# Kernel optimization log

Measured on AMD Instinct MI355X. Metric: run time of the kernel, lower is better.

Reference implementation:

```python
import jax, jax.numpy as jnp
import numpy as np

L, B, T, C, H, FF = 2, 2, 2048, 512, 8, 1024
HS = C // H  # head size
EPS = 1.1920929e-07  # torch float32 finfo eps (nn.RMSNorm default)


def setup_inputs() -> dict:
    key = jax.random.key(0)
    ks = jax.random.split(key, 20)
    s = 0.02
    return {
        "hidden": jax.random.normal(ks[0], (B, T, C), jnp.float32),
        "target": jax.random.normal(ks[1], (B, T, C), jnp.float32),
        # self-attn per-head projections (bias=False)
        "Wq_s": jax.random.normal(ks[2], (L, H, C, HS)) * s,
        "Wk_s": jax.random.normal(ks[3], (L, H, C, HS)) * s,
        "Wv_s": jax.random.normal(ks[4], (L, H, C, HS)) * s,
        "Wo_s": jax.random.normal(ks[5], (L, C, C)) * s,
        "bo_s": jnp.zeros((L, C)),
        # cross-attn per-head projections
        "Wq_x": jax.random.normal(ks[6], (L, H, C, HS)) * s,
        "Wk_x": jax.random.normal(ks[7], (L, H, C, HS)) * s,
        "Wv_x": jax.random.normal(ks[8], (L, H, C, HS)) * s,
        "Wo_x": jax.random.normal(ks[9], (L, C, C)) * s,
        "bo_x": jnp.zeros((L, C)),
        # FFN
        "W1": jax.random.normal(ks[10], (L, C, FF)) * s,
        "b1": jnp.zeros((L, FF)),
        "W2": jax.random.normal(ks[11], (L, FF, C)) * s,
        "b2": jnp.zeros((L, C)),
        # RMSNorm gains ln1..ln4
        "g1": jnp.ones((L, C)),
        "g2": jnp.ones((L, C)),
        "g3": jnp.ones((L, C)),
        "g4": jnp.ones((L, C)),
    }


def _rms(x, g):
    return x * jax.lax.rsqrt(jnp.mean(x * x, axis=-1, keepdims=True) + EPS) * g


def _attn(q_in, kv_in, Wq, Wk, Wv, Wo, bo, causal):
    # q_in: [B,Tq,C], kv_in: [B,Tk,C]; W*: [H,C,HS]
    q = jnp.einsum('btc,hcd->bhtd', q_in, Wq)
    k = jnp.einsum('bsc,hcd->bhsd', kv_in, Wk)
    v = jnp.einsum('bsc,hcd->bhsd', kv_in, Wv)
    wei = jnp.einsum('bhtd,bhsd->bhts', q, k) * (HS ** -0.5)  # [B,H,Tq,Tk]
    if causal:
        Tq, Tk = q_in.shape[1], kv_in.shape[1]
        mask = jnp.tril(jnp.ones((Tq, Tk), bool))
        wei = jnp.where(mask, wei, -jnp.inf)
    wei = jax.nn.softmax(wei, axis=-1)
    out = jnp.einsum('bhts,bhsd->bhtd', wei, v)
    out = out.transpose(0, 2, 1, 3).reshape(q_in.shape[0], q_in.shape[1], C)
    return out @ Wo + bo


def reference(hidden, target, Wq_s, Wk_s, Wv_s, Wo_s, bo_s,
              Wq_x, Wk_x, Wv_x, Wo_x, bo_x,
              W1, b1, W2, b2, g1, g2, g3, g4):
    t = target
    for l in range(L):
        # masked self-attention with RMSNorm pre-norm + residual
        t = t + _attn(_rms(t, g1[l]), _rms(t, g1[l]), Wq_s[l], Wk_s[l], Wv_s[l],
                      Wo_s[l], bo_s[l], causal=True)
        # cross-attention: K/V from ln2(hidden), Q from ln3(t)
        t = t + _attn(_rms(t, g3[l]), _rms(hidden, g2[l]), Wq_x[l], Wk_x[l], Wv_x[l],
                      Wo_x[l], bo_x[l], causal=False)
        # GELU FFN
        h = _rms(t, g4[l])
        t = t + (jax.nn.gelu(h @ W1[l] + b1[l], approximate=False) @ W2[l] + b2[l])
    return t
```

## Files before the change

### kernel.cpp

```cpp
#include <hip/hip_runtime.h>
#include <hip/hip_bf16.h>
#include <math.h>

#define L 2
#define B 2
#define T 2048
#define C 512
#define H 8
#define FF 1024
#define HS 64
#define EPSV 1.1920929e-07f

typedef __hip_bfloat16 bf16;
typedef __attribute__((ext_vector_type(8))) short short8;
typedef __attribute__((ext_vector_type(4))) float f32x4;

__device__ __forceinline__ float b2f(bf16 x) { return __bfloat162float(x); }

__device__ __forceinline__ void gl16(const unsigned short* g, unsigned short* l) {
    __builtin_amdgcn_global_load_lds(
        (const __attribute__((address_space(1))) unsigned int*)g,
        (__attribute__((address_space(3))) unsigned int*)l, 16, 0, 0);
}

__global__ void detect_k(const unsigned short* __restrict__ g1bits, int* __restrict__ flag) {
    if (threadIdx.x == 0 && blockIdx.x == 0)
        *flag = (g1bits[0] != (unsigned short)0x3F80u) ? 1 : 0;
}

__device__ __forceinline__ float ld_in(const void* p, size_t i, int fl) {
    return fl ? ((const float*)p)[i] : b2f(((const bf16*)p)[i]);
}

#define QKVT_TOT 1572864
#define WO_TOT 524288
#define W12_TOT 1048576
#define SM_TOT 9216
#define ACT_TOT 2097152
#define PREP_TOT (2 * QKVT_TOT + 2 * WO_TOT + 2 * W12_TOT + SM_TOT + 2 * ACT_TOT)

struct PrepArgs {
    const void *Wq_s, *Wk_s, *Wv_s, *Wo_s, *Wq_x, *Wk_x, *Wv_x, *Wo_x, *W1, *W2;
    const void* sm[8];
    const void *hidden, *target;
    bf16 *cQKVs, *cQKVx, *cWoTs, *cWoTx, *cW1T, *cW2T, *smallDst;
    float *hid, *t_buf;
    const int* flag;
};

__global__ void prep_k(PrepArgs pa) {
    long long i = (long long)blockIdx.x * 256 + threadIdx.x;
    if (i >= PREP_TOT) return;
    int fl = *pa.flag;
    if (i < 2LL * QKVT_TOT) {
        int which = i >= QKVT_TOT;
        int j = (int)(i - (long long)which * QKVT_TOT);
        int l = j / 786432, r = j - l * 786432;
        int n = r >> 9, c = r & 511;
        int p = n >> 9, nn = n & 511;
        int hh = nn >> 6, d = nn & 63;
        const void* src = which ? (p == 0 ? pa.Wq_x : p == 1 ? pa.Wk_x : pa.Wv_x)
                                : (p == 0 ? pa.Wq_s : p == 1 ? pa.Wk_s : pa.Wv_s);
        size_t si = ((size_t)(l * 8 + hh) * 512 + c) * 64 + d;
        (which ? pa.cQKVx : pa.cQKVs)[j] = __float2bfloat16(ld_in(src, si, fl));
        return;
    }
    i -= 2LL * QKVT_TOT;
    if (i < 2LL * WO_TOT) {
        int which = i >= WO_TOT;
        int j = (int)(i - (long long)which * WO_TOT);
        int l = j >> 18, r = j & 262143;
        int n = r >> 9, c = r & 511;
        size_t si = ((size_t)l << 18) + ((size_t)c << 9) + n;
        (which ? pa.cWoTx : pa.cWoTs)[j] = __float2bfloat16(ld_in(which ? pa.Wo_x : pa.Wo_s, si, fl));
        return;
    }
    i -= 2LL * WO_TOT;
    if (i < W12_TOT) {
        int j = (int)i;
        int l = j >> 19, r = j & 524287;
        int n = r >> 9, c = r & 511;
        size_t si = ((size_t)l << 19) + ((size_t)c << 10) + n;
        pa.cW1T[j] = __float2bfloat16(ld_in(pa.W1, si, fl));
        return;
    }
    i -= W12_TOT;
    if (i < W12_TOT) {
        int j = (int)i;
        int l = j >> 19, r = j & 524287;
        int n = r >> 10, c = r & 1023;
        size_t si = ((size_t)l << 19) + ((size_t)c << 9) + n;
        pa.cW2T[j] = __float2bfloat16(ld_in(pa.W2, si, fl));
        return;
    }
    i -= W12_TOT;
    if (i < SM_TOT) {
        int j = (int)i;
        const int cum[9] = {0, 1024, 2048, 4096, 5120, 6144, 7168, 8192, 9216};
        int k = 0;
        while (j >= cum[k + 1]) k++;
        pa.smallDst[j] = __float2bfloat16(ld_in(pa.sm[k], j - cum[k], fl));
        return;
    }
    i -= SM_TOT;
    if (i < ACT_TOT) {
        pa.hid[i] = ld_in(pa.hidden, (size_t)i, fl);
    } else {
        size_t j = i - ACT_TOT;
        pa.t_buf[j] = ld_in(pa.target, j, fl);
    }
}

__global__ void write_out_k(const float* __restrict__ in, void* __restrict__ out, int n,
                            const int* __restrict__ flag) {
    int i = blockIdx.x * blockDim.x + threadIdx.x;
    if (i >= n) return;
    if (*flag) ((float*)out)[i] = in[i];
    else       ((bf16*)out)[i] = __float2bfloat16(in[i]);
}

__global__ void rmsnorm_k(const float* __restrict__ x, const bf16* __restrict__ g,
                          bf16* __restrict__ y) {
    int row = blockIdx.x;
    int tid = threadIdx.x;
    const float* xr = x + (size_t)row * C;
    float v0 = xr[tid], v1 = xr[tid + 256];
    __shared__ float red[256];
    red[tid] = v0 * v0 + v1 * v1;
    __syncthreads();
    for (int s = 128; s > 0; s >>= 1) {
        if (tid < s) red[tid] += red[tid + s];
        __syncthreads();
    }
    float sc = rsqrtf(red[0] / (float)C + EPSV);
    y[(size_t)row * C + tid] = __float2bfloat16(v0 * sc * b2f(g[tid]));
    y[(size_t)row * C + tid + 256] = __float2bfloat16(v1 * sc * b2f(g[tid + 256]));
}

__global__ void rmsnorm2_k(const float* __restrict__ xa, const bf16* __restrict__ ga,
                           bf16* __restrict__ ya, const float* __restrict__ xb,
                           const bf16* __restrict__ gb, bf16* __restrict__ yb) {
    int sel = blockIdx.y;
    const float* x = sel ? xb : xa;
    const bf16* g = sel ? gb : ga;
    bf16* y = sel ? yb : ya;
    int row = blockIdx.x;
    int tid = threadIdx.x;
    const float* xr = x + (size_t)row * C;
    float v0 = xr[tid], v1 = xr[tid + 256];
    __shared__ float red[256];
    red[tid] = v0 * v0 + v1 * v1;
    __syncthreads();
    for (int s = 128; s > 0; s >>= 1) {
        if (tid < s) red[tid] += red[tid + s];
        __syncthreads();
    }
    float sc = rsqrtf(red[0] / (float)C + EPSV);
    y[(size_t)row * C + tid] = __float2bfloat16(v0 * sc * b2f(g[tid]));
    y[(size_t)row * C + tid + 256] = __float2bfloat16(v1 * sc * b2f(g[tid + 256]));
}

#define GPAD 40
struct GDesc {
    const bf16* A; const bf16* Bt; const bf16* bias; float* resid; bf16* out;
    int N, K, ldOut, ep, nblkx, blkofs;
};
struct GBatch { GDesc d[3]; int nd; };

__global__ __launch_bounds__(256) void gemm_batch_k(GBatch gb) {
    int bid = blockIdx.x;
    int di = 0;
    if (gb.nd > 1 && bid >= gb.d[1].blkofs) di = 1;
    if (gb.nd > 2 && bid >= gb.d[2].blkofs) di = 2;
    GDesc g = gb.d[di];
    int lb = bid - g.blkofs;
    int bx = lb % g.nblkx, by = lb / g.nblkx;
    int m0 = by * 64, n0 = bx * 64;

    __shared__ unsigned short As[2][64 * GPAD], Bs[2][64 * GPAD];
    int tid = threadIdx.x, lane = tid & 63, wave = tid >> 6;
    int wr = wave >> 1, wc = wave & 1, quad = lane >> 4, l15 = lane & 15;
    const unsigned short* Au = (const unsigned short*)g.A;
    const unsigned short* Bu = (const unsigned short*)g.Bt;

    int srow = tid >> 2;
    int sseg = tid & 3;
    const unsigned short* agp = Au + (size_t)(m0 + srow) * g.K + sseg * 8;
    const unsigned short* bgp = Bu + (size_t)(n0 + srow) * g.K + sseg * 8;
    int soff = srow * GPAD + sseg * 8;

    short8 va = *(const short8*)agp;
    short8 vb = *(const short8*)bgp;
    *(short8*)(&As[0][soff]) = va;
    *(short8*)(&Bs[0][soff]) = vb;

    f32x4 zf = {0.f, 0.f, 0.f, 0.f};
    f32x4 acc[2][2];
    acc[0][0] = zf; acc[0][1] = zf; acc[1][0] = zf; acc[1][1] = zf;

    int ra0 = wr * 32 + l15, ra1 = ra0 + 16;
    int rb0 = wc * 32 + l15, rb1 = rb0 + 16;
    int oa0 = ra0 * GPAD + quad * 8;
    int oa1 = ra1 * GPAD + quad * 8;
    int ob0 = rb0 * GPAD + quad * 8;
    int ob1 = rb1 * GPAD + quad * 8;

    int nk = g.K >> 5;
    __syncthreads();
    for (int kt = 0; kt < nk; kt++) {
        int cur = kt & 1;
        if (kt + 1 < nk) {
            va = *(const short8*)(agp + (kt + 1) * 32);
            vb = *(const short8*)(bgp + (kt + 1) * 32);
        }
        short8 a0 = *(const short8*)(&As[cur][oa0]);
        short8 a1 = *(const short8*)(&As[cur][oa1]);
        short8 b0 = *(const short8*)(&Bs[cur][ob0]);
        short8 b1 = *(const short8*)(&Bs[cur][ob1]);
        acc[0][0] = __builtin_amdgcn_mfma_f32_16x16x32_bf16(a0, b0, acc[0][0], 0, 0, 0);
        acc[0][1] = __builtin_amdgcn_mfma_f32_16x16x32_bf16(a0, b1, acc[0][1], 0, 0, 0);
        acc[1][0] = __builtin_amdgcn_mfma_f32_16x16x32_bf16(a1, b0, acc[1][0], 0, 0, 0);
        acc[1][1] = __builtin_amdgcn_mfma_f32_16x16x32_bf16(a1, b1, acc[1][1], 0, 0, 0);
        if (kt + 1 < nk) {
            *(short8*)(&As[cur ^ 1][soff]) = va;
            *(short8*)(&Bs[cur ^ 1][soff]) = vb;
        }
        __syncthreads();
    }

#pragma unroll
    for (int mi = 0; mi < 2; mi++) {
#pragma unroll
        for (int ni = 0; ni < 2; ni++) {
            int colg = n0 + wc * 32 + ni * 16 + l15;
            float bv = (g.ep == 1 || g.ep == 2) ? b2f(g.bias[colg]) : 0.f;
#pragma unroll
            for (int r2 = 0; r2 < 4; r2++) {
                int rowg = m0 + wr * 32 + mi * 16 + quad * 4 + r2;
                float v = acc[mi][ni][r2];
                if (g.ep == 0) {
                    g.out[(size_t)rowg * g.ldOut + colg] = __float2bfloat16(v);
                } else if (g.ep == 1) {
                    g.resid[(size_t)rowg * g.ldOut + colg] += v + bv;
                } else if (g.ep == 2) {
                    float u = v + bv;
                    g.out[(size_t)rowg * g.ldOut + colg] =
                        __float2bfloat16(0.5f * u * (1.f + erff(u * 0.70710678118654752f)));
                } else {
                    g.out[((size_t)((colg >> 11) * 512 + rowg) << 11) + (colg & 2047)] =
                        __float2bfloat16(v);
                }
            }
        }
    }
}

#define PST 72
__global__ __launch_bounds__(256) void attn_mfma_k(const bf16* __restrict__ qkv,
                                                   const bf16* __restrict__ vT,
                                                   bf16* __restrict__ attnout, int causal) {
    __shared__ unsigned short KsA[2][4096], VtA[2][4096];
    __shared__ unsigned short Ps[4][16 * PST];
    int qt = causal ? (gridDim.x - 1 - blockIdx.x) : blockIdx.x;
    int h = blockIdx.y, b = blockIdx.z;
    int tid = threadIdx.x, lane = tid & 63, w = tid >> 6;
    int quad = lane >> 4, l15 = lane & 15;
    const unsigned short* qk = (const unsigned short*)qkv;
    const unsigned short* vTp = (const unsigned short*)vT + ((size_t)b * 512 + h * 64) * T;
    size_t rowbase = (size_t)b * T;
    int koff = 512 + h * 64;
    unsigned short* Pw = Ps[w];
    bf16* Pwb = (bf16*)Pw;

    const unsigned short* qrow = qk + (rowbase + qt * 64 + w * 16 + l15) * 1536 + h * 64;
    short8 aq0 = *(const short8*)(qrow + quad * 8);
    short8 aq1 = *(const short8*)(qrow + 32 + quad * 8);

    int srow = lane >> 3;
    int ssp = (lane & 7) ^ (srow & 7);

    f32x4 zf = {0.f, 0.f, 0.f, 0.f};
    f32x4 oacc[4];
#pragma unroll
    for (int i = 0; i < 4; i++) oacc[i] = zf;
    float lpart[4] = {0.f, 0.f, 0.f, 0.f};

    int nT = causal ? (qt + 1) : (T / 64);

#pragma unroll
    for (int j = 0; j < 2; j++) {
        int c = w * 2 + j;
        int r = c * 8 + srow;
        gl16(qk + (rowbase + r) * 1536 + koff + ssp * 8, KsA[0] + c * 512);
        gl16(vTp + (size_t)r * T + ssp * 8, VtA[0] + c * 512);
    }
    __syncthreads();

    int buf = 0;
    for (int st = 0; st < nT; st++) {
        if (st + 1 < nT) {
#pragma unroll
            for (int j = 0; j < 2; j++) {
                int c = w * 2 + j;
                int r = c * 8 + srow;
                gl16(qk + (rowbase + (st + 1) * 64 + r) * 1536 + koff + ssp * 8,
                     KsA[buf ^ 1] + c * 512);
                gl16(vTp + (size_t)r * T + (st + 1) * 64 + ssp * 8, VtA[buf ^ 1] + c * 512);
            }
        }

        const unsigned short* Kb = KsA[buf];
        const unsigned short* Vb = VtA[buf];

        f32x4 sacc[4];
#pragma unroll
        for (int i = 0; i < 4; i++) sacc[i] = zf;
#pragma unroll
        for (int ni = 0; ni < 4; ni++) {
            int rr = ni * 16 + l15;
            short8 bk0 = *(const short8*)(Kb + rr * 64 + ((quad ^ (rr & 7)) * 8));
            short8 bk1 = *(const short8*)(Kb + rr * 64 + (((4 + quad) ^ (rr & 7)) * 8));
            sacc[ni] = __builtin_amdgcn_mfma_f32_16x16x32_bf16(aq0, bk0, sacc[ni], 0, 0, 0);
            sacc[ni] = __builtin_amdgcn_mfma_f32_16x16x32_bf16(aq1, bk1, sacc[ni], 0, 0, 0);
        }

        bool diag = causal && (st == qt);
        int qrl = w * 16 + quad * 4;
#pragma unroll
        for (int reg = 0; reg < 4; reg++) {
            float lp = 0.f;
#pragma unroll
            for (int ni = 0; ni < 4; ni++) {
                int s_l = ni * 16 + l15;
                float p = __expf(sacc[ni][reg] * 0.125f);
                if (diag && s_l > qrl + reg) p = 0.f;
                lp += p;
                Pwb[(quad * 4 + reg) * PST + s_l] = __float2bfloat16(p);
            }
            lpart[reg] += lp;
        }

        short8 ap0 = *(const short8*)(Pw + l15 * PST + quad * 8);
        short8 ap1 = *(const short8*)(Pw + l15 * PST + 32 + quad * 8);
#pragma unroll
        for (int dj = 0; dj < 4; dj++) {
            int rr = dj * 16 + l15;
            short8 bv0 = *(const short8*)(Vb + rr * 64 + ((quad ^ (rr & 7)) * 8));
            short8 bv1 = *(const short8*)(Vb + rr * 64 + (((4 + quad) ^ (rr & 7)) * 8));
            oacc[dj] = __builtin_amdgcn_mfma_f32_16x16x32_bf16(ap0, bv0, oacc[dj], 0, 0, 0);
            oacc[dj] = __builtin_amdgcn_mfma_f32_16x16x32_bf16(ap1, bv1, oacc[dj], 0, 0, 0);
        }

        __syncthreads();
        buf ^= 1;
    }

#pragma unroll
    for (int reg = 0; reg < 4; reg++) {
#pragma unroll
        for (int mk = 1; mk < 16; mk <<= 1) lpart[reg] += __shfl_xor(lpart[reg], mk, 64);
        lpart[reg] = 1.0f / lpart[reg];
    }
#pragma unroll
    for (int dj = 0; dj < 4; dj++) {
        int d = dj * 16 + l15;
#pragma unroll
        for (int reg = 0; reg < 4; reg++) {
            int q = w * 16 + quad * 4 + reg;
            attnout[(rowbase + qt * 64 + q) * C + h * HS + d] =
                __float2bfloat16(oacc[dj][reg] * lpart[reg]);
        }
    }
}

extern "C" void kernel_launch(void* const* d_in, const int* in_sizes, int n_in,
                              void* d_out, int out_size, void* d_ws, size_t ws_size,
                              hipStream_t stream) {
    const int BTC = B * T * C;
    const int BTF = B * T * FF;

    char* wsb = (char*)d_ws;
    int* flag = (int*)wsb;
    bf16* cur = (bf16*)(wsb + 256);
    bf16* cQKVs = cur;   cur += QKVT_TOT;
    bf16* cQKVx = cur;   cur += QKVT_TOT;
    bf16* cWoTs = cur;   cur += WO_TOT;
    bf16* cWoTx = cur;   cur += WO_TOT;
    bf16* cW1T = cur;    cur += W12_TOT;
    bf16* cW2T = cur;    cur += W12_TOT;
    bf16* smallBase = cur;
    bf16* cbo_s = cur;   cur += L * C;
    bf16* cbo_x = cur;   cur += L * C;
    bf16* cb1 = cur;     cur += L * FF;
    bf16* cb2 = cur;     cur += L * C;
    bf16* cg1 = cur;     cur += L * C;
    bf16* cg2 = cur;     cur += L * C;
    bf16* cg3 = cur;     cur += L * C;
    bf16* cg4 = cur;     cur += L * C;
    bf16* n1 = cur;      cur += BTC;
    bf16* n2 = cur;      cur += BTC;
    bf16* qkvbuf = cur;  cur += B * T * 3 * C;
    bf16* vTbuf = cur;   cur += BTC;
    bf16* attnout = cur; cur += BTC;
    bf16* h1buf = cur;   cur += BTF;
    size_t f32_off = (((char*)cur - wsb) + 255) & ~(size_t)255;
    float* t_buf = (float*)(wsb + f32_off);
    float* hid = t_buf + BTC;

    dim3 blk256(256);
    detect_k<<<1, 64, 0, stream>>>((const unsigned short*)d_in[16], flag);

    PrepArgs pa;
    pa.Wq_s = d_in[2]; pa.Wk_s = d_in[3]; pa.Wv_s = d_in[4]; pa.Wo_s = d_in[5];
    pa.Wq_x = d_in[7]; pa.Wk_x = d_in[8]; pa.Wv_x = d_in[9]; pa.Wo_x = d_in[10];
    pa.W1 = d_in[12]; pa.W2 = d_in[14];
    pa.sm[0] = d_in[6];  pa.sm[1] = d_in[11]; pa.sm[2] = d_in[13]; pa.sm[3] = d_in[15];
    pa.sm[4] = d_in[16]; pa.sm[5] = d_in[17]; pa.sm[6] = d_in[18]; pa.sm[7] = d_in[19];
    pa.hidden = d_in[0]; pa.target = d_in[1];
    pa.cQKVs = cQKVs; pa.cQKVx = cQKVx; pa.cWoTs = cWoTs; pa.cWoTx = cWoTx;
    pa.cW1T = cW1T; pa.cW2T = cW2T; pa.smallDst = smallBase;
    pa.hid = hid; pa.t_buf = t_buf; pa.flag = flag;
    prep_k<<<(PREP_TOT + 255) / 256, blk256, 0, stream>>>(pa);

    const int M = B * T;
    dim3 attngrid(T / 64, H, B);

    for (int l = 0; l < L; l++) {
        bf16* qkvW_s = cQKVs + (size_t)l * 3 * C * C;
        bf16* qkvW_x = cQKVx + (size_t)l * 3 * C * C;
        bf16* woT_s = cWoTs + (size_t)l * C * C;
        bf16* woT_x = cWoTx + (size_t)l * C * C;
        bf16* w1T = cW1T + (size_t)l * C * FF;
        bf16* w2T = cW2T + (size_t)l * FF * C;

        rmsnorm_k<<<M, blk256, 0, stream>>>(t_buf, cg1 + l * C, n1);
        {
            GBatch gb;
            gb.nd = 2;
            gb.d[0] = {n1, qkvW_s, nullptr, nullptr, qkvbuf, 1024, C, 3 * C, 0, 16, 0};
            gb.d[1] = {qkvW_s + (size_t)1024 * C, n1, nullptr, nullptr, vTbuf,
                       M, C, 0, 3, 64, 1024};
            gemm_batch_k<<<1024 + 512, blk256, 0, stream>>>(gb);
        }
        attn_mfma_k<<<attngrid, blk256, 0, stream>>>(qkvbuf, vTbuf, attnout, 1);
        {
            GBatch gb;
            gb.nd = 1;
            gb.d[0] = {attnout, woT_s, cbo_s + l * C, t_buf, nullptr, C, C, C, 1, 8, 0};
            gemm_batch_k<<<512, blk256, 0, stream>>>(gb);
        }

        rmsnorm2_k<<<dim3(M, 2), blk256, 0, stream>>>(t_buf, cg3 + l * C, n1, hid, cg2 + l * C, n2);
        {
            GBatch gb;
            gb.nd = 3;
            gb.d[0] = {n1, qkvW_x, nullptr, nullptr, qkvbuf, C, C, 3 * C, 0, 8, 0};
            gb.d[1] = {n2, qkvW_x + (size_t)512 * C, nullptr, nullptr, qkvbuf + C,
                       C, C, 3 * C, 0, 8, 512};
            gb.d[2] = {qkvW_x + (size_t)1024 * C, n2, nullptr, nullptr, vTbuf,
                       M, C, 0, 3, 64, 1024};
            gemm_batch_k<<<512 + 512 + 512, blk256, 0, stream>>>(gb);
        }
        attn_mfma_k<<<attngrid, blk256, 0, stream>>>(qkvbuf, vTbuf, attnout, 0);
        {
            GBatch gb;
            gb.nd = 1;
            gb.d[0] = {attnout, woT_x, cbo_x + l * C, t_buf, nullptr, C, C, C, 1, 8, 0};
            gemm_batch_k<<<512, blk256, 0, stream>>>(gb);
        }

        rmsnorm_k<<<M, blk256, 0, stream>>>(t_buf, cg4 + l * C, n1);
        {
            GBatch gb;
            gb.nd = 1;
            gb.d[0] = {n1, w1T, cb1 + l * FF, nullptr, h1buf, FF, C, FF, 2, 16, 0};
            gemm_batch_k<<<1024, blk256, 0, stream>>>(gb);
        }
        {
            GBatch gb;
            gb.nd = 1;
            gb.d[0] = {h1buf, w2T, cb2 + l * C, t_buf, nullptr, C, FF, C, 1, 8, 0};
            gemm_batch_k<<<512, blk256, 0, stream>>>(gb);
        }
    }

    write_out_k<<<(BTC + 255) / 256, blk256, 0, stream>>>(t_buf, d_out, BTC, flag);
}
```

Before: 550.6 us.

## Enlarge GEMM tiles to 128x128 with direct-to-LDS loads and XOR swizzle

Replaces the 64x64 GEMM kernel with a 128x128 tile version. Each wave now computes a 4x4 grid of 16x16 MFMA tiles, which raises operand reuse per LDS read. Global tiles are streamed into double-buffered LDS with global_load_lds instead of passing through registers, and an XOR swizzle replaces the padding used to avoid bank conflicts. The trade-off is that the launch grids shrink sharply: some GEMMs now launch only 128 blocks, which leaves many CUs idle on a large GPU, and each thread holds more accumulator registers.

Measured after the change: 690.3 us. 1.25x slower.

```diff
diff --git a/kernel.cpp b/kernel.cpp
--- a/kernel.cpp
+++ b/kernel.cpp
@@ -160,14 +160,13 @@
     y[(size_t)row * C + tid + 256] = __float2bfloat16(v1 * sc * b2f(g[tid + 256]));
 }
 
-#define GPAD 40
 struct GDesc {
     const bf16* A; const bf16* Bt; const bf16* bias; float* resid; bf16* out;
     int N, K, ldOut, ep, nblkx, blkofs;
 };
 struct GBatch { GDesc d[3]; int nd; };
 
-__global__ __launch_bounds__(256) void gemm_batch_k(GBatch gb) {
+__global__ __launch_bounds__(256) void gemm128_k(GBatch gb) {
     int bid = blockIdx.x;
     int di = 0;
     if (gb.nd > 1 && bid >= gb.d[1].blkofs) di = 1;
@@ -175,68 +174,77 @@
     GDesc g = gb.d[di];
     int lb = bid - g.blkofs;
     int bx = lb % g.nblkx, by = lb / g.nblkx;
-    int m0 = by * 64, n0 = bx * 64;
-
-    __shared__ unsigned short As[2][64 * GPAD], Bs[2][64 * GPAD];
+    int m0 = by * 128, n0 = bx * 128;
+
+    __shared__ alignas(16) unsigned short As[2][128 * 32];
+    __shared__ alignas(16) unsigned short Bs[2][128 * 32];
     int tid = threadIdx.x, lane = tid & 63, wave = tid >> 6;
     int wr = wave >> 1, wc = wave & 1, quad = lane >> 4, l15 = lane & 15;
     const unsigned short* Au = (const unsigned short*)g.A;
     const unsigned short* Bu = (const unsigned short*)g.Bt;
 
-    int srow = tid >> 2;
-    int sseg = tid & 3;
-    const unsigned short* agp = Au + (size_t)(m0 + srow) * g.K + sseg * 8;
-    const unsigned short* bgp = Bu + (size_t)(n0 + srow) * g.K + sseg * 8;
-    int soff = srow * GPAD + sseg * 8;
-
-    short8 va = *(const short8*)agp;
-    short8 vb = *(const short8*)bgp;
-    *(short8*)(&As[0][soff]) = va;
-    *(short8*)(&Bs[0][soff]) = vb;
+    int r0 = tid >> 2, sp0 = tid & 3;
+    int gs0 = sp0 ^ (r0 & 3);
+    const unsigned short* agp0 = Au + (size_t)(m0 + r0) * g.K + gs0 * 8;
+    const unsigned short* agp1 = Au + (size_t)(m0 + r0 + 64) * g.K + gs0 * 8;
+    const unsigned short* bgp0 = Bu + (size_t)(n0 + r0) * g.K + gs0 * 8;
+    const unsigned short* bgp1 = Bu + (size_t)(n0 + r0 + 64) * g.K + gs0 * 8;
+    int wofs = wave * 512;
 
     f32x4 zf = {0.f, 0.f, 0.f, 0.f};
-    f32x4 acc[2][2];
-    acc[0][0] = zf; acc[0][1] = zf; acc[1][0] = zf; acc[1][1] = zf;
-
-    int ra0 = wr * 32 + l15, ra1 = ra0 + 16;
-    int rb0 = wc * 32 + l15, rb1 = rb0 + 16;
-    int oa0 = ra0 * GPAD + quad * 8;
-    int oa1 = ra1 * GPAD + quad * 8;
-    int ob0 = rb0 * GPAD + quad * 8;
-    int ob1 = rb1 * GPAD + quad * 8;
+    f32x4 acc[4][4];
+#pragma unroll
+    for (int i = 0; i < 4; i++)
+#pragma unroll
+        for (int j = 0; j < 4; j++) acc[i][j] = zf;
+
+    int sw8 = (quad ^ (l15 & 3)) * 8;
+    int arow = wr * 64 + l15, brow = wc * 64 + l15;
 
     int nk = g.K >> 5;
+    {
+        gl16(agp0, &As[0][wofs]);
+        gl16(agp1, &As[0][wofs + 2048]);
+        gl16(bgp0, &Bs[0][wofs]);
+        gl16(bgp1, &Bs[0][wofs + 2048]);
+    }
     __syncthreads();
+    int buf = 0;
     for (int kt = 0; kt < nk; kt++) {
-        int cur = kt & 1;
         if (kt + 1 < nk) {
-            va = *(const short8*)(agp + (kt + 1) * 32);
-            vb = *(const short8*)(bgp + (kt + 1) * 32);
-        }
-        short8 a0 = *(const short8*)(&As[cur][oa0]);
-        short8 a1 = *(const short8*)(&As[cur][oa1]);
-        short8 b0 = *(const short8*)(&Bs[cur][ob0]);
-        short8 b1 = *(const short8*)(&Bs[cur][ob1]);
-        acc[0][0] = __builtin_amdgcn_mfma_f32_16x16x32_bf16(a0, b0, acc[0][0], 0, 0, 0);
-        acc[0][1] = __builtin_amdgcn_mfma_f32_16x16x32_bf16(a0, b1, acc[0][1], 0, 0, 0);
-        acc[1][0] = __builtin_amdgcn_mfma_f32_16x16x32_bf16(a1, b0, acc[1][0], 0, 0, 0);
-        acc[1][1] = __builtin_amdgcn_mfma_f32_16x16x32_bf16(a1, b1, acc[1][1], 0, 0, 0);
-        if (kt + 1 < nk) {
-            *(short8*)(&As[cur ^ 1][soff]) = va;
-            *(short8*)(&Bs[cur ^ 1][soff]) = vb;
-        }
+        int ko = (kt + 1) << 5;
+            gl16(agp0 + ko, &As[buf ^ 1][wofs]);
+            gl16(agp1 + ko, &As[buf ^ 1][wofs + 2048]);
+            gl16(bgp0 + ko, &Bs[buf ^ 1][wofs]);
+            gl16(bgp1 + ko, &Bs[buf ^ 1][wofs + 2048]);
+        }
+        const unsigned short* Ab = As[buf];
+        const unsigned short* Bb = Bs[buf];
+        short8 af[4], bg[4];
+#pragma unroll
+        for (int i = 0; i < 4; i++) {
+            af[i] = *(const short8*)(Ab + ((arow + i * 16) << 5) + sw8);
+            bg[i] = *(const short8*)(Bb + ((brow + i * 16) << 5) + sw8);
+        }
+#pragma unroll
+        for (int mi = 0; mi < 4; mi++)
+#pragma unroll
+            for (int ni = 0; ni < 4; ni++)
+                acc[mi][ni] =
+                    __builtin_amdgcn_mfma_f32_16x16x32_bf16(af[mi], bg[ni], acc[mi][ni], 0, 0, 0);
         __syncthreads();
-    }
-
-#pragma unroll
-    for (int mi = 0; mi < 2; mi++) {
-#pragma unroll
-        for (int ni = 0; ni < 2; ni++) {
-            int colg = n0 + wc * 32 + ni * 16 + l15;
+        buf ^= 1;
+    }
+
+#pragma unroll
+    for (int mi = 0; mi < 4; mi++) {
+#pragma unroll
+        for (int ni = 0; ni < 4; ni++) {
+            int colg = n0 + wc * 64 + ni * 16 + l15;
             float bv = (g.ep == 1 || g.ep == 2) ? b2f(g.bias[colg]) : 0.f;
 #pragma unroll
             for (int r2 = 0; r2 < 4; r2++) {
-                int rowg = m0 + wr * 32 + mi * 16 + quad * 4 + r2;
+                int rowg = m0 + wr * 64 + mi * 16 + quad * 4 + r2;
                 float v = acc[mi][ni][r2];
                 if (g.ep == 0) {
                     g.out[(size_t)rowg * g.ldOut + colg] = __float2bfloat16(v);
@@ -437,50 +445,50 @@
         {
             GBatch gb;
             gb.nd = 2;
-            gb.d[0] = {n1, qkvW_s, nullptr, nullptr, qkvbuf, 1024, C, 3 * C, 0, 16, 0};
+            gb.d[0] = {n1, qkvW_s, nullptr, nullptr, qkvbuf, 1024, C, 3 * C, 0, 8, 0};
             gb.d[1] = {qkvW_s + (size_t)1024 * C, n1, nullptr, nullptr, vTbuf,
-                       M, C, 0, 3, 64, 1024};
-            gemm_batch_k<<<1024 + 512, blk256, 0, stream>>>(gb);
+                       M, C, 0, 3, 32, 256};
+            gemm128_k<<<256 + 128, blk256, 0, stream>>>(gb);
         }
         attn_mfma_k<<<attngrid, blk256, 0, stream>>>(qkvbuf, vTbuf, attnout, 1);
         {
             GBatch gb;
             gb.nd = 1;
-            gb.d[0] = {attnout, woT_s, cbo_s + l * C, t_buf, nullptr, C, C, C, 1, 8, 0};
-            gemm_batch_k<<<512, blk256, 0, stream>>>(gb);
+            gb.d[0] = {attnout, woT_s, cbo_s + l * C, t_buf, nullptr, C, C, C, 1, 4, 0};
+            gemm128_k<<<128, blk256, 0, stream>>>(gb);
         }
 
         rmsnorm2_k<<<dim3(M, 2), blk256, 0, stream>>>(t_buf, cg3 + l * C, n1, hid, cg2 + l * C, n2);
         {
             GBatch gb;
             gb.nd = 3;
-            gb.d[0] = {n1, qkvW_x, nullptr, nullptr, qkvbuf, C, C, 3 * C, 0, 8, 0};
+            gb.d[0] = {n1, qkvW_x, nullptr, nullptr, qkvbuf, C, C, 3 * C, 0, 4, 0};
             gb.d[1] = {n2, qkvW_x + (size_t)512 * C, nullptr, nullptr, qkvbuf + C,
-                       C, C, 3 * C, 0, 8, 512};
+                       C, C, 3 * C, 0, 4, 128};
             gb.d[2] = {qkvW_x + (size_t)1024 * C, n2, nullptr, nullptr, vTbuf,
-                       M, C, 0, 3, 64, 1024};
-            gemm_batch_k<<<512 + 512 + 512, blk256, 0, stream>>>(gb);
+                       M, C, 0, 3, 32, 256};
+            gemm128_k<<<128 + 128 + 128, blk256, 0, stream>>>(gb);
         }
         attn_mfma_k<<<attngrid, blk256, 0, stream>>>(qkvbuf, vTbuf, attnout, 0);
         {
             GBatch gb;
             gb.nd = 1;
-            gb.d[0] = {attnout, woT_x, cbo_x + l * C, t_buf, nullptr, C, C, C, 1, 8, 0};
-            gemm_batch_k<<<512, blk256, 0, stream>>>(gb);
+            gb.d[0] = {attnout, woT_x, cbo_x + l * C, t_buf, nullptr, C, C, C, 1, 4, 0};
+            gemm128_k<<<128, blk256, 0, stream>>>(gb);
         }
 
         rmsnorm_k<<<M, blk256, 0, stream>>>(t_buf, cg4 + l * C, n1);
         {
             GBatch gb;
             gb.nd = 1;
-            gb.d[0] = {n1, w1T, cb1 + l * FF, nullptr, h1buf, FF, C, FF, 2, 16, 0};
-            gemm_batch_k<<<1024, blk256, 0, stream>>>(gb);
+            gb.d[0] = {n1, w1T, cb1 + l * FF, nullptr, h1buf, FF, C, FF, 2, 8, 0};
+            gemm128_k<<<256, blk256, 0, stream>>>(gb);
         }
         {
             GBatch gb;
             gb.nd = 1;
-            gb.d[0] = {h1buf, w2T, cb2 + l * C, t_buf, nullptr, C, FF, C, 1, 8, 0};
-            gemm_batch_k<<<512, blk256, 0, stream>>>(gb);
+            gb.d[0] = {h1buf, w2T, cb2 + l * C, t_buf, nullptr, C, FF, C, 1, 4, 0};
+            gemm128_k<<<128, blk256, 0, stream>>>(gb);
         }
     }
 
```

## Use direct global-to-LDS loads with XOR-swizzled layout and BK=64 in GEMM

Applied to the files above, without the earlier changes.

Rewrites the GEMM main loop to load tiles with global_load_lds directly into shared memory instead of staging through registers. The padded LDS layout is replaced by an XOR swizzle to avoid bank conflicts, and the K-tile doubles from 32 to 64, so each barrier covers two MFMAs per accumulator. The goal is fewer VGPRs and load instructions and fewer syncs per K. The trade-off is larger LDS use (32KB), which may lower occupancy.

New measurement: 527.2 us. 4.2% less time.

```diff
diff --git a/kernel.cpp b/kernel.cpp
--- a/kernel.cpp
+++ b/kernel.cpp
@@ -160,14 +160,13 @@
     y[(size_t)row * C + tid + 256] = __float2bfloat16(v1 * sc * b2f(g[tid + 256]));
 }
 
-#define GPAD 40
 struct GDesc {
     const bf16* A; const bf16* Bt; const bf16* bias; float* resid; bf16* out;
     int N, K, ldOut, ep, nblkx, blkofs;
 };
 struct GBatch { GDesc d[3]; int nd; };
 
-__global__ __launch_bounds__(256) void gemm_batch_k(GBatch gb) {
+__global__ __launch_bounds__(256) void gemm64_k(GBatch gb) {
     int bid = blockIdx.x;
     int di = 0;
     if (gb.nd > 1 && bid >= gb.d[1].blkofs) di = 1;
@@ -177,55 +176,68 @@
     int bx = lb % g.nblkx, by = lb / g.nblkx;
     int m0 = by * 64, n0 = bx * 64;
 
-    __shared__ unsigned short As[2][64 * GPAD], Bs[2][64 * GPAD];
+    __shared__ alignas(16) unsigned short As[2][64 * 64];
+    __shared__ alignas(16) unsigned short Bs[2][64 * 64];
     int tid = threadIdx.x, lane = tid & 63, wave = tid >> 6;
     int wr = wave >> 1, wc = wave & 1, quad = lane >> 4, l15 = lane & 15;
     const unsigned short* Au = (const unsigned short*)g.A;
     const unsigned short* Bu = (const unsigned short*)g.Bt;
 
-    int srow = tid >> 2;
-    int sseg = tid & 3;
-    const unsigned short* agp = Au + (size_t)(m0 + srow) * g.K + sseg * 8;
-    const unsigned short* bgp = Bu + (size_t)(n0 + srow) * g.K + sseg * 8;
-    int soff = srow * GPAD + sseg * 8;
-
-    short8 va = *(const short8*)agp;
-    short8 vb = *(const short8*)bgp;
-    *(short8*)(&As[0][soff]) = va;
-    *(short8*)(&Bs[0][soff]) = vb;
+    int r0 = tid >> 3, sg = tid & 7;
+    int gs = sg ^ (r0 & 7);
+    const unsigned short* agp0 = Au + (size_t)(m0 + r0) * g.K + gs * 8;
+    const unsigned short* agp1 = Au + (size_t)(m0 + r0 + 32) * g.K + gs * 8;
+    const unsigned short* bgp0 = Bu + (size_t)(n0 + r0) * g.K + gs * 8;
+    const unsigned short* bgp1 = Bu + (size_t)(n0 + r0 + 32) * g.K + gs * 8;
+    int wofs = wave * 512;
 
     f32x4 zf = {0.f, 0.f, 0.f, 0.f};
     f32x4 acc[2][2];
     acc[0][0] = zf; acc[0][1] = zf; acc[1][0] = zf; acc[1][1] = zf;
 
-    int ra0 = wr * 32 + l15, ra1 = ra0 + 16;
-    int rb0 = wc * 32 + l15, rb1 = rb0 + 16;
-    int oa0 = ra0 * GPAD + quad * 8;
-    int oa1 = ra1 * GPAD + quad * 8;
-    int ob0 = rb0 * GPAD + quad * 8;
-    int ob1 = rb1 * GPAD + quad * 8;
-
-    int nk = g.K >> 5;
+    int sws0 = ((quad) ^ (l15 & 7)) * 8;
+    int sws1 = ((4 + quad) ^ (l15 & 7)) * 8;
+    int arow = wr * 32 + l15, brow = wc * 32 + l15;
+
+    int nk = g.K >> 6;
+    {
+        gl16(agp0, &As[0][wofs]);
+        gl16(agp1, &As[0][wofs + 2048]);
+        gl16(bgp0, &Bs[0][wofs]);
+        gl16(bgp1, &Bs[0][wofs + 2048]);
+    }
     __syncthreads();
+    int buf = 0;
     for (int kt = 0; kt < nk; kt++) {
-        int cur = kt & 1;
         if (kt + 1 < nk) {
-            va = *(const short8*)(agp + (kt + 1) * 32);
-            vb = *(const short8*)(bgp + (kt + 1) * 32);
-        }
-        short8 a0 = *(const short8*)(&As[cur][oa0]);
-        short8 a1 = *(const short8*)(&As[cur][oa1]);
-        short8 b0 = *(const short8*)(&Bs[cur][ob0]);
-        short8 b1 = *(const short8*)(&Bs[cur][ob1]);
-        acc[0][0] = __builtin_amdgcn_mfma_f32_16x16x32_bf16(a0, b0, acc[0][0], 0, 0, 0);
-        acc[0][1] = __builtin_amdgcn_mfma_f32_16x16x32_bf16(a0, b1, acc[0][1], 0, 0, 0);
-        acc[1][0] = __builtin_amdgcn_mfma_f32_16x16x32_bf16(a1, b0, acc[1][0], 0, 0, 0);
-        acc[1][1] = __builtin_amdgcn_mfma_f32_16x16x32_bf16(a1, b1, acc[1][1], 0, 0, 0);
-        if (kt + 1 < nk) {
-            *(short8*)(&As[cur ^ 1][soff]) = va;
-            *(short8*)(&Bs[cur ^ 1][soff]) = vb;
-        }
+            int ko = (kt + 1) << 6;
+            gl16(agp0 + ko, &As[buf ^ 1][wofs]);
+            gl16(agp1 + ko, &As[buf ^ 1][wofs + 2048]);
+            gl16(bgp0 + ko, &Bs[buf ^ 1][wofs]);
+            gl16(bgp1 + ko, &Bs[buf ^ 1][wofs + 2048]);
+        }
+        const unsigned short* Ab = As[buf];
+        const unsigned short* Bb = Bs[buf];
+        short8 a0[2], b0[2], a1[2], b1[2];
+#pragma unroll
+        for (int i = 0; i < 2; i++) {
+            int ra = (arow + i * 16) << 6, rb = (brow + i * 16) << 6;
+            a0[i] = *(const short8*)(Ab + ra + sws0);
+            a1[i] = *(const short8*)(Ab + ra + sws1);
+            b0[i] = *(const short8*)(Bb + rb + sws0);
+            b1[i] = *(const short8*)(Bb + rb + sws1);
+        }
+#pragma unroll
+        for (int mi = 0; mi < 2; mi++)
+#pragma unroll
+            for (int ni = 0; ni < 2; ni++) {
+                acc[mi][ni] =
+                    __builtin_amdgcn_mfma_f32_16x16x32_bf16(a0[mi], b0[ni], acc[mi][ni], 0, 0, 0);
+                acc[mi][ni] =
+                    __builtin_amdgcn_mfma_f32_16x16x32_bf16(a1[mi], b1[ni], acc[mi][ni], 0, 0, 0);
+            }
         __syncthreads();
+        buf ^= 1;
     }
 
 #pragma unroll
@@ -440,14 +452,14 @@
             gb.d[0] = {n1, qkvW_s, nullptr, nullptr, qkvbuf, 1024, C, 3 * C, 0, 16, 0};
             gb.d[1] = {qkvW_s + (size_t)1024 * C, n1, nullptr, nullptr, vTbuf,
                        M, C, 0, 3, 64, 1024};
-            gemm_batch_k<<<1024 + 512, blk256, 0, stream>>>(gb);
+            gemm64_k<<<1024 + 512, blk256, 0, stream>>>(gb);
         }
         attn_mfma_k<<<attngrid, blk256, 0, stream>>>(qkvbuf, vTbuf, attnout, 1);
         {
             GBatch gb;
             gb.nd = 1;
             gb.d[0] = {attnout, woT_s, cbo_s + l * C, t_buf, nullptr, C, C, C, 1, 8, 0};
-            gemm_batch_k<<<512, blk256, 0, stream>>>(gb);
+            gemm64_k<<<512, blk256, 0, stream>>>(gb);
         }
 
         rmsnorm2_k<<<dim3(M, 2), blk256, 0, stream>>>(t_buf, cg3 + l * C, n1, hid, cg2 + l * C, n2);
@@ -459,14 +471,14 @@
                        C, C, 3 * C, 0, 8, 512};
             gb.d[2] = {qkvW_x + (size_t)1024 * C, n2, nullptr, nullptr, vTbuf,
                        M, C, 0, 3, 64, 1024};
-            gemm_batch_k<<<512 + 512 + 512, blk256, 0, stream>>>(gb);
+            gemm64_k<<<512 + 512 + 512, blk256, 0, stream>>>(gb);
         }
         attn_mfma_k<<<attngrid, blk256, 0, stream>>>(qkvbuf, vTbuf, attnout, 0);
         {
             GBatch gb;
             gb.nd = 1;
             gb.d[0] = {attnout, woT_x, cbo_x + l * C, t_buf, nullptr, C, C, C, 1, 8, 0};
-            gemm_batch_k<<<512, blk256, 0, stream>>>(gb);
+            gemm64_k<<<512, blk256, 0, stream>>>(gb);
         }
 
         rmsnorm_k<<<M, blk256, 0, stream>>>(t_buf, cg4 + l * C, n1);
@@ -474,13 +486,13 @@
             GBatch gb;
             gb.nd = 1;
             gb.d[0] = {n1, w1T, cb1 + l * FF, nullptr, h1buf, FF, C, FF, 2, 16, 0};
-            gemm_batch_k<<<1024, blk256, 0, stream>>>(gb);
+            gemm64_k<<<1024, blk256, 0, stream>>>(gb);
         }
         {
             GBatch gb;
             gb.nd = 1;
             gb.d[0] = {h1buf, w2T, cb2 + l * C, t_buf, nullptr, C, FF, C, 1, 8, 0};
-            gemm_batch_k<<<512, blk256, 0, stream>>>(gb);
+            gemm64_k<<<512, blk256, 0, stream>>>(gb);
         }
     }
 
```
